# Optimization experiments

Hardware: AMD Instinct MI355X
Metric: run time of the kernel (lower is better)

Reference implementation:

```python
import jax, jax.numpy as jnp
import numpy as np

B, N, D, H, DP, DC = 1, 768, 768, 12, 128, 512
DH = D // H

def _ln(x, eps=1e-5):
    m = jnp.mean(x, axis=-1, keepdims=True)
    v = jnp.mean((x - m) ** 2, axis=-1, keepdims=True)
    return (x - m) * jax.lax.rsqrt(v + eps)

def setup_inputs() -> dict:
    key = jax.random.key(0)
    ks = jax.random.split(key, 12)
    w = lambda k, shape: jax.random.normal(k, shape, jnp.float32) * 0.02
    return dict(
        x=jax.random.normal(ks[0], (B, N, D), jnp.float32),
        pair_rep=jax.random.normal(ks[1], (B, N, N, DP), jnp.float32),
        cond=jax.random.normal(ks[2], (B, N, DC), jnp.float32),
        adaln_cond_gamma=jnp.ones((DC,), jnp.float32),
        adaln_cond_beta=jnp.zeros((DC,), jnp.float32),
        adaln_Wg=w(ks[3], (DC, D)),
        adaln_bg=jnp.zeros((D,), jnp.float32),
        adaln_Wb=w(ks[4], (DC, D)),
        Wq=w(ks[5], (D, D)), bq=jnp.zeros((D,), jnp.float32),
        Wk=w(ks[6], (D, D)), bk=jnp.zeros((D,), jnp.float32),
        Wv=w(ks[7], (D, D)), bv=jnp.zeros((D,), jnp.float32),
        qln_g=jnp.ones((DH,), jnp.float32), qln_b=jnp.zeros((DH,), jnp.float32),
        kln_g=jnp.ones((DH,), jnp.float32), kln_b=jnp.zeros((DH,), jnp.float32),
        pair_ln_g=jnp.ones((DP,), jnp.float32), pair_ln_b=jnp.zeros((DP,), jnp.float32),
        W_pair_bias=w(ks[8], (DP, H)),
        Wo=w(ks[9], (D, D)), bo=jnp.zeros((D,), jnp.float32),
        scale_W=w(ks[10], (DC, D)),
        scale_b=jnp.full((D,), -2.0, jnp.float32),  # adaLN-zero style gate bias
        mask=jnp.ones((B, N), jnp.bool_),
    )

def reference(x, pair_rep, cond, adaln_cond_gamma, adaln_cond_beta, adaln_Wg, adaln_bg,
              adaln_Wb, Wq, bq, Wk, bk, Wv, bv, qln_g, qln_b, kln_g, kln_b,
              pair_ln_g, pair_ln_b, W_pair_bias, Wo, bo, scale_W, scale_b, mask):
    b, n, d = x.shape
    mf = mask.astype(x.dtype)                      # [b, n]
    pair_mask = mf[:, :, None] * mf[:, None, :]    # [b, n, n]
    # --- AdaptiveLayerNorm: LN(x) modulated by conditioning ---
    cn = _ln(cond) * adaln_cond_gamma + adaln_cond_beta
    h = _ln(x) * jax.nn.sigmoid(cn @ adaln_Wg + adaln_bg) + cn @ adaln_Wb
    h = h * mf[..., None]
    # --- PairBiasAttention ---
    q = (h @ Wq + bq).reshape(b, n, H, DH)
    k = (h @ Wk + bk).reshape(b, n, H, DH)
    v = (h @ Wv + bv).reshape(b, n, H, DH)
    q = _ln(q) * qln_g + qln_b                     # per-head QK layernorm
    k = _ln(k) * kln_g + kln_b
    bias = (_ln(pair_rep) * pair_ln_g + pair_ln_b) @ W_pair_bias  # [b, n, n, H]
    scores = jnp.einsum('bihd,bjhd->bhij', q, k) * (1.0 / np.sqrt(DH).astype(np.float32))
    scores = scores + bias.transpose(0, 3, 1, 2)
    scores = jnp.where(pair_mask[:, None, :, :] > 0, scores, jnp.float32(-1e9))
    attn = jax.nn.softmax(scores, axis=-1)
    o = jnp.einsum('bhij,bjhd->bihd', attn, v).reshape(b, n, d)
    o = o @ Wo + bo
    # --- AdaptiveLayerNormOutputScale + final mask ---
    o = o * jax.nn.sigmoid(cond @ scale_W + scale_b) * mf[..., None]
    return o * mf[..., None]
```

## Files before the change

### kernel.cpp

```cpp
#include <hip/hip_runtime.h>
#include <math.h>

#define NN 768
#define DD 768
#define NHEAD 12
#define DPAIR 128
#define DCOND 512

typedef unsigned short u16;
typedef unsigned int u32;
typedef __attribute__((ext_vector_type(8))) short s8v;
typedef __attribute__((ext_vector_type(4))) float f4v;
#define MFMA __builtin_amdgcn_mfma_f32_16x16x32_bf16

__device__ inline u16 bf16_rne(float x) {
    u32 u = __float_as_uint(x);
    u32 r = (u + 0x7FFFu + ((u >> 16) & 1u)) >> 16;
    return (u16)r;
}
__device__ inline float bf16_f(u16 h) { return __uint_as_float(((u32)h) << 16); }
__device__ inline void split_bf16(float x, u16& hi, u16& lo) {
    hi = bf16_rne(x);
    lo = bf16_rne(x - bf16_f(hi));
}
__device__ inline u32 pk2(float a, float b) {
    return (u32)bf16_rne(a) | ((u32)bf16_rne(b) << 16);
}

struct PrepP {
    const float *pg, *pb, *Wpb, *bq, *bk, *bv, *cond, *cg, *cb, *x;
    const float* w768in[4];
    const float* w512in[3];
    u16* WpT;
    float *Av, *Bv, *bias3, *xn;
    u16 *w768oh[4], *w768ol[4], *w512oh[3], *w512ol[3];
    u16 *cnh, *cnl, *condh, *condl;
};

__device__ __forceinline__ void dev_wprep(const float* in, u16* oh, u16* ol, int K, int N,
                                          int k0, int n0) {
    __shared__ float ls[64][65];
    int t = threadIdx.x, rr = t >> 4, c4 = (t & 15) * 4;
#pragma unroll
    for (int ph = 0; ph < 4; ph++) {
        int row = ph * 16 + rr;
        float4 v = *(const float4*)(in + (long)(k0 + row) * N + n0 + c4);
        ls[c4 + 0][row] = v.x; ls[c4 + 1][row] = v.y;
        ls[c4 + 2][row] = v.z; ls[c4 + 3][row] = v.w;
    }
    __syncthreads();
#pragma unroll
    for (int ph = 0; ph < 4; ph++) {
        int row = ph * 16 + rr;
        u16 h4[4], l4[4];
#pragma unroll
        for (int i = 0; i < 4; i++) split_bf16(ls[row][c4 + i], h4[i], l4[i]);
        u32 ha = (u32)h4[0] | ((u32)h4[1] << 16), hb = (u32)h4[2] | ((u32)h4[3] << 16);
        u32 la = (u32)l4[0] | ((u32)l4[1] << 16), lb = (u32)l4[2] | ((u32)l4[3] << 16);
        long ob = (long)(n0 + row) * K + k0 + c4;
        *(uint2*)(oh + ob) = make_uint2(ha, hb);
        *(uint2*)(ol + ob) = make_uint2(la, lb);
    }
}

__device__ __forceinline__ void dev_rowln(const float* in, int C, int row,
                                          const float* g, const float* b, float* outf,
                                          u16* oh, u16* ol, u16* rawh, u16* rawl) {
    const float* x = in + (size_t)row * C;
    int t = threadIdx.x;
    float s = 0.f, s2 = 0.f;
    for (int c = t; c < C; c += 256) { float v = x[c]; s += v; s2 += v * v; }
    for (int o = 32; o > 0; o >>= 1) { s += __shfl_xor(s, o); s2 += __shfl_xor(s2, o); }
    __shared__ float r0[4], r1[4];
    int wid = t >> 6, lane = t & 63;
    if (lane == 0) { r0[wid] = s; r1[wid] = s2; }
    __syncthreads();
    s = r0[0] + r0[1] + r0[2] + r0[3];
    s2 = r1[0] + r1[1] + r1[2] + r1[3];
    float m = s / C, var = s2 / C - m * m;
    float r = rsqrtf(var + 1e-5f);
    for (int c = t; c < C; c += 256) {
        float xv = x[c];
        float v = (xv - m) * r;
        if (g) v = v * g[c] + b[c];
        size_t idx = (size_t)row * C + c;
        if (outf) outf[idx] = v;
        if (oh) { u16 hi, lo; split_bf16(v, hi, lo); oh[idx] = hi; ol[idx] = lo; }
        if (rawh) { u16 hi, lo; split_bf16(xv, hi, lo); rawh[idx] = hi; rawl[idx] = lo; }
    }
}

__global__ __launch_bounds__(256) void k_prep_all(PrepP p) {
    int bid = blockIdx.x;
    if (bid == 0) {
        int t = threadIdx.x;
        if (t < DPAIR) {
            float g = p.pg[t];
#pragma unroll
            for (int h = 0; h < 16; h++) {
                float w = (h < 12) ? g * p.Wpb[t * NHEAD + h] : 0.f;
                p.WpT[h * DPAIR + t] = bf16_rne(w);
            }
        }
        for (int idx = t; idx < 3 * DD; idx += 256) {
            float v = (idx < DD) ? p.bq[idx] : (idx < 2 * DD) ? p.bk[idx - DD] : p.bv[idx - 2 * DD];
            p.bias3[idx] = v;
        }
        if (t < NHEAD) {
            float a = 0.f, b = 0.f;
            for (int c = 0; c < DPAIR; c++) {
                a += p.pg[c] * p.Wpb[c * NHEAD + t];
                b += p.pb[c] * p.Wpb[c * NHEAD + t];
            }
            p.Av[t] = a; p.Bv[t] = b;
        }
    } else if (bid <= 576) {
        int i = bid - 1;
        dev_wprep(p.w768in[i / 144], p.w768oh[i / 144], p.w768ol[i / 144], 768, 768,
                  (i % 12) * 64, ((i / 12) % 12) * 64);
    } else if (bid <= 864) {
        int i = bid - 577;
        dev_wprep(p.w512in[i / 96], p.w512oh[i / 96], p.w512ol[i / 96], 512, 768,
                  (i & 7) * 64, ((i >> 3) % 12) * 64);
    } else if (bid <= 1632) {
        int row = bid - 865;
        dev_rowln(p.cond, 512, row, p.cg, p.cb, nullptr, p.cnh, p.cnl, p.condh, p.condl);
    } else {
        int row = bid - 1633;
        dev_rowln(p.x, 768, row, nullptr, nullptr, p.xn, nullptr, nullptr, nullptr, nullptr);
    }
}

__global__ __launch_bounds__(256) void k_pair2(const float* __restrict__ pr,
                                               const u16* __restrict__ WpT,
                                               const float* __restrict__ Av, const float* __restrict__ Bv,
                                               float* __restrict__ S) {
    __shared__ u16 At[64][128];
    __shared__ float mrow[64], rrow[64];
    long row0 = (long)blockIdx.x * 64;
    int t = threadIdx.x;
    int r = t >> 2, q = t & 3;
    const float* src = pr + (row0 + r) * DPAIR + q * 32;
    float4 v[8];
#pragma unroll
    for (int i = 0; i < 8; i++) v[i] = *(const float4*)(src + i * 4);
    float s = 0.f, s2 = 0.f;
#pragma unroll
    for (int i = 0; i < 8; i++) {
        s += v[i].x + v[i].y + v[i].z + v[i].w;
        s2 = fmaf(v[i].x, v[i].x, s2); s2 = fmaf(v[i].y, v[i].y, s2);
        s2 = fmaf(v[i].z, v[i].z, s2); s2 = fmaf(v[i].w, v[i].w, s2);
    }
    s += __shfl_xor(s, 1); s2 += __shfl_xor(s2, 1);
    s += __shfl_xor(s, 2); s2 += __shfl_xor(s2, 2);
    if (q == 0) {
        float m = s * (1.f / 128.f);
        float var = s2 * (1.f / 128.f) - m * m;
        mrow[r] = m; rrow[r] = rsqrtf(var + 1e-5f);
    }
#pragma unroll
    for (int i2 = 0; i2 < 4; i2++) {
        uint4 pk = make_uint4(pk2(v[i2 * 2].x, v[i2 * 2].y), pk2(v[i2 * 2].z, v[i2 * 2].w),
                              pk2(v[i2 * 2 + 1].x, v[i2 * 2 + 1].y), pk2(v[i2 * 2 + 1].z, v[i2 * 2 + 1].w));
        int byte = (q * 64 + i2 * 16) ^ ((r & 7) << 4);
        *(uint4*)((char*)&At[r][0] + byte) = pk;
    }
    __syncthreads();
    int w = t >> 6, l = t & 63, fr = l & 15, fq = l >> 4;
    float Ah = (fr < 12) ? Av[fr] : 0.f;
    float Bh = (fr < 12) ? Bv[fr] : 0.f;
    f4v acc = {};
#pragma unroll
    for (int ks = 0; ks < 4; ks++) {
        int arow = w * 16 + fr;
        s8v a = *(const s8v*)((char*)&At[arow][0] + ((ks * 64 + fq * 16) ^ ((arow & 7) << 4)));
        s8v b = *(const s8v*)(WpT + fr * DPAIR + ks * 32 + fq * 8);
        acc = MFMA(a, b, acc, 0, 0, 0);
    }
    if (fr < 12) {
#pragma unroll
        for (int rr = 0; rr < 4; rr++) {
            int gr = w * 16 + fq * 4 + rr;
            float bias = rrow[gr] * (acc[rr] - mrow[gr] * Ah) + Bh;
            S[(size_t)fr * (NN * NN) + row0 + gr] = bias;
        }
    }
}

__device__ __forceinline__ void gemm_phase(const u16* __restrict__ Ahp, const u16* __restrict__ Alp,
                                           const u16* __restrict__ Bhp, const u16* __restrict__ Blp,
                                           int nk, u16 (*At)[64][32], u16 (*Bt)[64][32],
                                           f4v (*acc)[2], int r, int sl, int wm, int wn,
                                           int fr, int fk) {
    uint4 ra = *(const uint4*)Ahp, rb = *(const uint4*)Alp;
    uint4 rc = *(const uint4*)Bhp, rd = *(const uint4*)Blp;
    for (int ks = 0; ks < nk; ks++) {
        *(uint4*)&At[0][r][sl * 8] = ra;
        *(uint4*)&At[1][r][sl * 8] = rb;
        *(uint4*)&Bt[0][r][sl * 8] = rc;
        *(uint4*)&Bt[1][r][sl * 8] = rd;
        __syncthreads();
        if (ks + 1 < nk) {
            int ko = (ks + 1) * 32;
            ra = *(const uint4*)(Ahp + ko); rb = *(const uint4*)(Alp + ko);
            rc = *(const uint4*)(Bhp + ko); rd = *(const uint4*)(Blp + ko);
        }
        s8v ah0 = *(const s8v*)&At[0][wm + fr][fk];
        s8v ah1 = *(const s8v*)&At[0][wm + 16 + fr][fk];
        s8v al0 = *(const s8v*)&At[1][wm + fr][fk];
        s8v al1 = *(const s8v*)&At[1][wm + 16 + fr][fk];
        s8v bh0 = *(const s8v*)&Bt[0][wn + fr][fk];
        s8v bh1 = *(const s8v*)&Bt[0][wn + 16 + fr][fk];
        s8v bl0 = *(const s8v*)&Bt[1][wn + fr][fk];
        s8v bl1 = *(const s8v*)&Bt[1][wn + 16 + fr][fk];
        acc[0][0] = MFMA(ah0, bh0, acc[0][0], 0, 0, 0);
        acc[0][0] = MFMA(ah0, bl0, acc[0][0], 0, 0, 0);
        acc[0][0] = MFMA(al0, bh0, acc[0][0], 0, 0, 0);
        acc[0][1] = MFMA(ah0, bh1, acc[0][1], 0, 0, 0);
        acc[0][1] = MFMA(ah0, bl1, acc[0][1], 0, 0, 0);
        acc[0][1] = MFMA(al0, bh1, acc[0][1], 0, 0, 0);
        acc[1][0] = MFMA(ah1, bh0, acc[1][0], 0, 0, 0);
        acc[1][0] = MFMA(ah1, bl0, acc[1][0], 0, 0, 0);
        acc[1][0] = MFMA(al1, bh0, acc[1][0], 0, 0, 0);
        acc[1][1] = MFMA(ah1, bh1, acc[1][1], 0, 0, 0);
        acc[1][1] = MFMA(ah1, bl1, acc[1][1], 0, 0, 0);
        acc[1][1] = MFMA(al1, bh1, acc[1][1], 0, 0, 0);
        __syncthreads();
    }
}

__global__ __launch_bounds__(256, 2) void k_adaln_gemm(const u16* __restrict__ Ah_, const u16* __restrict__ Al_,
                                                       const u16* __restrict__ Bgh_, const u16* __restrict__ Bgl_,
                                                       const u16* __restrict__ Bbh_, const u16* __restrict__ Bbl_,
                                                       const float* __restrict__ xn, const float* __restrict__ bg,
                                                       u16* __restrict__ hh, u16* __restrict__ hl) {
    __shared__ u16 Aa[2][64][32];
    __shared__ u16 Bb[4][64][32];
    int t = threadIdx.x;
    int m0 = blockIdx.x * 64, n0 = blockIdx.y * 64;
    int r = t >> 2, sl = t & 3;
    const u16* ap0 = Ah_ + (long)(m0 + r) * DCOND + sl * 8;
    const u16* ap1 = Al_ + (long)(m0 + r) * DCOND + sl * 8;
    const u16* bp0 = Bgh_ + (long)(n0 + r) * DCOND + sl * 8;
    const u16* bp1 = Bgl_ + (long)(n0 + r) * DCOND + sl * 8;
    const u16* bp2 = Bbh_ + (long)(n0 + r) * DCOND + sl * 8;
    const u16* bp3 = Bbl_ + (long)(n0 + r) * DCOND + sl * 8;
    int l = t & 63, w = t >> 6;
    int wm = (w >> 1) * 32, wn = (w & 1) * 32;
    int fr = l & 15, fq = l >> 4, fk = fq * 8;
    f4v ag[2][2] = {}, ab[2][2] = {};
    uint4 ra = *(const uint4*)ap0, rb = *(const uint4*)ap1;
    uint4 rc = *(const uint4*)bp0, rd = *(const uint4*)bp1;
    uint4 re = *(const uint4*)bp2, rf = *(const uint4*)bp3;
    for (int ks = 0; ks < 16; ks++) {
        *(uint4*)&Aa[0][r][sl * 8] = ra;
        *(uint4*)&Aa[1][r][sl * 8] = rb;
        *(uint4*)&Bb[0][r][sl * 8] = rc;
        *(uint4*)&Bb[1][r][sl * 8] = rd;
        *(uint4*)&Bb[2][r][sl * 8] = re;
        *(uint4*)&Bb[3][r][sl * 8] = rf;
        __syncthreads();
        if (ks + 1 < 16) {
            int ko = (ks + 1) * 32;
            ra = *(const uint4*)(ap0 + ko); rb = *(const uint4*)(ap1 + ko);
            rc = *(const uint4*)(bp0 + ko); rd = *(const uint4*)(bp1 + ko);
            re = *(const uint4*)(bp2 + ko); rf = *(const uint4*)(bp3 + ko);
        }
        s8v ah0 = *(const s8v*)&Aa[0][wm + fr][fk];
        s8v ah1 = *(const s8v*)&Aa[0][wm + 16 + fr][fk];
        s8v al0 = *(const s8v*)&Aa[1][wm + fr][fk];
        s8v al1 = *(const s8v*)&Aa[1][wm + 16 + fr][fk];
        s8v gh0 = *(const s8v*)&Bb[0][wn + fr][fk];
        s8v gh1 = *(const s8v*)&Bb[0][wn + 16 + fr][fk];
        s8v gl0 = *(const s8v*)&Bb[1][wn + fr][fk];
        s8v gl1 = *(const s8v*)&Bb[1][wn + 16 + fr][fk];
        s8v bh0 = *(const s8v*)&Bb[2][wn + fr][fk];
        s8v bh1 = *(const s8v*)&Bb[2][wn + 16 + fr][fk];
        s8v bl0 = *(const s8v*)&Bb[3][wn + fr][fk];
        s8v bl1 = *(const s8v*)&Bb[3][wn + 16 + fr][fk];
        ag[0][0] = MFMA(ah0, gh0, ag[0][0], 0, 0, 0);
        ag[0][0] = MFMA(ah0, gl0, ag[0][0], 0, 0, 0);
        ag[0][0] = MFMA(al0, gh0, ag[0][0], 0, 0, 0);
        ag[0][1] = MFMA(ah0, gh1, ag[0][1], 0, 0, 0);
        ag[0][1] = MFMA(ah0, gl1, ag[0][1], 0, 0, 0);
        ag[0][1] = MFMA(al0, gh1, ag[0][1], 0, 0, 0);
        ag[1][0] = MFMA(ah1, gh0, ag[1][0], 0, 0, 0);
        ag[1][0] = MFMA(ah1, gl0, ag[1][0], 0, 0, 0);
        ag[1][0] = MFMA(al1, gh0, ag[1][0], 0, 0, 0);
        ag[1][1] = MFMA(ah1, gh1, ag[1][1], 0, 0, 0);
        ag[1][1] = MFMA(ah1, gl1, ag[1][1], 0, 0, 0);
        ag[1][1] = MFMA(al1, gh1, ag[1][1], 0, 0, 0);
        ab[0][0] = MFMA(ah0, bh0, ab[0][0], 0, 0, 0);
        ab[0][0] = MFMA(ah0, bl0, ab[0][0], 0, 0, 0);
        ab[0][0] = MFMA(al0, bh0, ab[0][0], 0, 0, 0);
// ... 11 lines not shown
#pragma unroll
    for (int mi = 0; mi < 2; mi++)
#pragma unroll
        for (int ni = 0; ni < 2; ni++)
#pragma unroll
            for (int rr = 0; rr < 4; rr++) {
                long row = m0 + wm + mi * 16 + fq * 4 + rr;
                int col = n0 + wn + ni * 16 + fr;
                float gate = 1.f / (1.f + __expf(-(ag[mi][ni][rr] + bg[col])));
                float hv = xn[row * DD + col] * gate + ab[mi][ni][rr];
                u16 hi, lo; split_bf16(hv, hi, lo);
                hh[row * DD + col] = hi; hl[row * DD + col] = lo;
            }
}

__global__ __launch_bounds__(256, 2) void k_qkv_gemm(const u16* __restrict__ Ah_, const u16* __restrict__ Al_,
                                                     const u16* __restrict__ Wh, const u16* __restrict__ Wl,
                                                     const float* __restrict__ bias3,
                                                     const float* __restrict__ gq, const float* __restrict__ bqv,
                                                     const float* __restrict__ gk, const float* __restrict__ bkv,
                                                     u16* __restrict__ qh, u16* __restrict__ ql,
                                                     u16* __restrict__ kh, u16* __restrict__ vth) {
    __shared__ u16 At[2][64][32], Bt[2][64][32];
    __shared__ float redS[2][64], redS2[2][64];
    int t = threadIdx.x;
    int m0 = blockIdx.x * 64, n0 = blockIdx.y * 64, z = blockIdx.z;
    int r = t >> 2, sl = t & 3;
    const u16* Ahp = Ah_ + (long)(m0 + r) * DD + sl * 8;
    const u16* Alp = Al_ + (long)(m0 + r) * DD + sl * 8;
    const u16* Bhp = Wh + (long)z * 589824 + (long)(n0 + r) * DD + sl * 8;
    const u16* Blp = Wl + (long)z * 589824 + (long)(n0 + r) * DD + sl * 8;
    int l = t & 63, w = t >> 6;
    int wm = (w >> 1) * 32, wn = (w & 1) * 32;
    int fr = l & 15, fq = l >> 4, fk = fq * 8;
    f4v acc[2][2] = {};
    gemm_phase(Ahp, Alp, Bhp, Blp, 24, At, Bt, acc, r, sl, wm, wn, fr, fk);
    float vv[2][2][4];
#pragma unroll
    for (int mi = 0; mi < 2; mi++)
#pragma unroll
        for (int ni = 0; ni < 2; ni++)
#pragma unroll
            for (int rr = 0; rr < 4; rr++)
                vv[mi][ni][rr] = acc[mi][ni][rr] + bias3[z * DD + n0 + wn + ni * 16 + fr];
    if (z == 2) {
#pragma unroll
        for (int mi = 0; mi < 2; mi++)
#pragma unroll
            for (int ni = 0; ni < 2; ni++)
#pragma unroll
                for (int rr = 0; rr < 4; rr++) {
// ... 4 lines not shown
        return;
    }
    int wi = w & 1;
#pragma unroll
    for (int mi = 0; mi < 2; mi++)
#pragma unroll
        for (int rr = 0; rr < 4; rr++) {
            float sv = vv[mi][0][rr] + vv[mi][1][rr];
            float s2v = vv[mi][0][rr] * vv[mi][0][rr] + vv[mi][1][rr] * vv[mi][1][rr];
            sv += __shfl_xor(sv, 1); s2v += __shfl_xor(s2v, 1);
            sv += __shfl_xor(sv, 2); s2v += __shfl_xor(s2v, 2);
            sv += __shfl_xor(sv, 4); s2v += __shfl_xor(s2v, 4);
            sv += __shfl_xor(sv, 8); s2v += __shfl_xor(s2v, 8);
            if (fr == 0) {
                int row = wm + mi * 16 + fq * 4 + rr;
                redS[wi][row] = sv; redS2[wi][row] = s2v;
            }
        }
    __syncthreads();
    const float* g = z ? gk : gq;
    const float* bb = z ? bkv : bqv;
    float scale = z ? 1.f : 0.125f;
#pragma unroll
    for (int mi = 0; mi < 2; mi++)
#pragma unroll
        for (int ni = 0; ni < 2; ni++)
#pragma unroll
            for (int rr = 0; rr < 4; rr++) {
                int row = wm + mi * 16 + fq * 4 + rr;
                float m = (redS[0][row] + redS[1][row]) * (1.f / 64.f);
                float var = (redS2[0][row] + redS2[1][row]) * (1.f / 64.f) - m * m;
                float rs = rsqrtf(var + 1e-5f);
                int colh = wn + ni * 16 + fr;
                float y = ((vv[mi][ni][rr] - m) * rs * g[colh] + bb[colh]) * scale;
                size_t idx = (size_t)(m0 + row) * DD + n0 + colh;
                if (z == 0) { u16 hi, lo; split_bf16(y, hi, lo); qh[idx] = hi; ql[idx] = lo; }
                else kh[idx] = bf16_rne(y);
            }
}

__global__ __launch_bounds__(128) void k_flash(const u16* __restrict__ qh, const u16* __restrict__ ql,
                                               const u16* __restrict__ kh, const u16* __restrict__ vt,
                                               const float* __restrict__ S,
                                               u16* __restrict__ oh, u16* __restrict__ ol) {
    __shared__ u16 Kt[64][64];
    __shared__ u16 Vt[64][64];
    __shared__ u16 Pt[2][16][72];
    int i0 = blockIdx.x * 32, h = blockIdx.y;
    int t = threadIdx.x, w = t >> 6, l = t & 63, fr = l & 15, fq = l >> 4;
    const u16* qsrc = qh + (size_t)(i0 + w * 16 + fr) * DD + h * 64 + fq * 8;
    const u16* qsrc2 = ql + (size_t)(i0 + w * 16 + fr) * DD + h * 64 + fq * 8;
    s8v qa0 = *(const s8v*)qsrc, qa1 = *(const s8v*)(qsrc + 32);
    s8v qb0 = *(const s8v*)qsrc2, qb1 = *(const s8v*)(qsrc2 + 32);
// ... 29 lines not shown
            sc[nf] = MFMA(qb0, kb0, sc[nf], 0, 0, 0);
            sc[nf] = MFMA(qa1, kb1, sc[nf], 0, 0, 0);
            sc[nf] = MFMA(qb1, kb1, sc[nf], 0, 0, 0);
        }
#pragma unroll
        for (int rr = 0; rr < 4; rr++) {
            float mx = fmaxf(fmaxf(sc[0][rr], sc[1][rr]), fmaxf(sc[2][rr], sc[3][rr]));
            mx = fmaxf(mx, __shfl_xor(mx, 1));
            mx = fmaxf(mx, __shfl_xor(mx, 2));
            mx = fmaxf(mx, __shfl_xor(mx, 4));
            mx = fmaxf(mx, __shfl_xor(mx, 8));
            float mnew = fmaxf(mrun[rr], mx);
            float ps = 0.f;
#pragma unroll
            for (int nf = 0; nf < 4; nf++) {
                float p = __expf(sc[nf][rr] - mnew);
                sc[nf][rr] = p;
                ps += p;
            }
            ps += __shfl_xor(ps, 1); ps += __shfl_xor(ps, 2);
            ps += __shfl_xor(ps, 4); ps += __shfl_xor(ps, 8);
            float f = __expf(mrun[rr] - mnew);
            lrun[rr] = lrun[rr] * f + ps;
            mrun[rr] = mnew;
#pragma unroll
            for (int nf = 0; nf < 4; nf++) Oacc[nf][rr] *= f;
        }
#pragma unroll
        for (int nf = 0; nf < 4; nf++)
#pragma unroll
            for (int rr = 0; rr < 4; rr++)
                Pt[w][fq * 4 + rr][nf * 16 + fr] = bf16_rne(sc[nf][rr]);
#pragma unroll
// ... 7 lines not shown
            }
        }
        __syncthreads();
    }
#pragma unroll
    for (int rr = 0; rr < 4; rr++) lrun[rr] = 1.f / lrun[rr];
#pragma unroll
    for (int nf = 0; nf < 4; nf++)
#pragma unroll
        for (int rr = 0; rr < 4; rr++) {
            float o = Oacc[nf][rr] * lrun[rr];
            u16 hi, lo; split_bf16(o, hi, lo);
            size_t idx = (size_t)(i0 + w * 16 + fq * 4 + rr) * DD + h * 64 + nf * 16 + fr;
            oh[idx] = hi; ol[idx] = lo;
        }
}

__global__ __launch_bounds__(256, 2) void k_out_gemm(const u16* __restrict__ oh_, const u16* __restrict__ ol_,
                                                     const u16* __restrict__ Woh, const u16* __restrict__ Wol,
                                                     const u16* __restrict__ ch, const u16* __restrict__ cl,
                                                     const u16* __restrict__ sWh, const u16* __restrict__ sWl,
                                                     const float* __restrict__ bo, const float* __restrict__ sb,
                                                     float* __restrict__ outp) {
    __shared__ u16 At[2][64][32], Bt[2][64][32];
    int t = threadIdx.x;
    int m0 = blockIdx.x * 64, n0 = blockIdx.y * 64;
    int r = t >> 2, sl = t & 3;
    int l = t & 63, w = t >> 6;
    int wm = (w >> 1) * 32, wn = (w & 1) * 32;
    int fr = l & 15, fq = l >> 4, fk = fq * 8;
// ... 62 lines not shown
    u16* condl = up; up += E5;
    u16* hh = up; up += E;
    u16* hl = up; up += E;
    u16* qh = up; up += E;
    u16* ql = up; up += E;
    u16* kh = up; up += E;
    u16* vth = up; up += E;
    u16* WT768h = up; up += 4 * E;
    u16* WT768l = up; up += 4 * E;
    u16* WT512h = up; up += 3 * E5;
    u16* WT512l = up; up += 3 * E5;
    u16* WpT = up; up += 2048;

    float* out = (float*)d_out;

    PrepP P;
    P.pg = pg; P.pb = pb; P.Wpb = Wpb; P.bq = bq; P.bk = bk; P.bv = bv;
    P.cond = cond; P.cg = cg; P.cb = cb; P.x = x;
    P.w768in[0] = Wq; P.w768in[1] = Wk; P.w768in[2] = Wv; P.w768in[3] = Wo;
    P.w512in[0] = Wg; P.w512in[1] = Wb; P.w512in[2] = sW;
    P.WpT = WpT; P.Av = Av; P.Bv = Bv; P.bias3 = bias3; P.xn = xn;
    for (int i = 0; i < 4; i++) { P.w768oh[i] = WT768h + i * E; P.w768ol[i] = WT768l + i * E; }
    for (int i = 0; i < 3; i++) { P.w512oh[i] = WT512h + i * E5; P.w512ol[i] = WT512l + i * E5; }
    P.cnh = cnh; P.cnl = cnl; P.condh = condh; P.condl = condl;

    k_prep_all<<<2401, 256, 0, stream>>>(P);
    k_pair2<<<9216, 256, 0, stream>>>(pair, WpT, Av, Bv, S);
    k_adaln_gemm<<<dim3(12, 12), 256, 0, stream>>>(cnh, cnl, WT512h, WT512l,
                                                   WT512h + E5, WT512l + E5, xn, bg, hh, hl);
    k_qkv_gemm<<<dim3(12, 12, 3), 256, 0, stream>>>(hh, hl, WT768h, WT768l, bias3,
                                                    qln_g, qln_b, kln_g, kln_b, qh, ql, kh, vth);
    k_flash<<<dim3(24, 12), 128, 0, stream>>>(qh, ql, kh, vth, S, qh, ql);
    k_out_gemm<<<dim3(12, 12), 256, 0, stream>>>(qh, ql, WT768h + 3 * E, WT768l + 3 * E,
                                                 condh, condl, WT512h + 2 * E5, WT512l + 2 * E5,
                                                 bo, sb, out);
}
```

Measured before the change: 213.4 us.

## Co-schedule pair-bias blocks with prep, adaLN and QKV GEMM launches

The 9216 pair-bias blocks are split across three fused launches (1800, 3400 and 4016 blocks). Each share runs alongside the weight-prep/LN stage, the adaLN GEMM and the QKV GEMM, using block-index dispatch and a shared-memory union. The aim is to fill idle compute units during the small GEMM launches with bandwidth-heavy pair work, and to drop one kernel launch. It adds a tiny separate prep0 launch that must finish first. Launch bounds of 2 blocks per SM and the larger shared-memory union may reduce occupancy for the pair blocks.

Result: faster. 189.9 us (-11.0%).

```diff
diff --git a/kernel.cpp b/kernel.cpp
--- a/kernel.cpp
+++ b/kernel.cpp
@@ -27,26 +27,99 @@
     return (u32)bf16_rne(a) | ((u32)bf16_rne(b) << 16);
 }
 
-struct PrepP {
-    const float *pg, *pb, *Wpb, *bq, *bk, *bv, *cond, *cg, *cb, *x;
-    const float* w768in[4];
-    const float* w512in[3];
-    u16* WpT;
-    float *Av, *Bv, *bias3, *xn;
-    u16 *w768oh[4], *w768ol[4], *w512oh[3], *w512ol[3];
-    u16 *cnh, *cnl, *condh, *condl;
-};
+struct SmPair { u16 At[64][128]; float mrow[64]; float rrow[64]; };
+struct SmW    { float ls[64][65]; float r0[4]; float r1[4]; };
+struct SmAda  { u16 Aa[2][64][32]; u16 Bb[4][64][32]; };
+struct SmQkv  { u16 At[2][64][32]; u16 Bt[2][64][32]; float redS[2][64]; float redS2[2][64]; };
+
+__global__ void k_prep0(const float* __restrict__ pg, const float* __restrict__ pb,
+                        const float* __restrict__ W, u16* __restrict__ WpT,
+                        float* __restrict__ Av, float* __restrict__ Bv,
+                        const float* __restrict__ bq, const float* __restrict__ bk,
+                        const float* __restrict__ bv, float* __restrict__ bias3) {
+    int t = threadIdx.x;
+    if (t < DPAIR) {
+        float g = pg[t];
+#pragma unroll
+        for (int h = 0; h < 16; h++) {
+            float w = (h < 12) ? g * W[t * NHEAD + h] : 0.f;
+            WpT[h * DPAIR + t] = bf16_rne(w);
+        }
+    }
+    for (int idx = t; idx < 3 * DD; idx += 256) {
+        float v = (idx < DD) ? bq[idx] : (idx < 2 * DD) ? bk[idx - DD] : bv[idx - 2 * DD];
+        bias3[idx] = v;
+    }
+    if (t < NHEAD) {
+        float a = 0.f, b = 0.f;
+        for (int c = 0; c < DPAIR; c++) { a += pg[c] * W[c * NHEAD + t]; b += pb[c] * W[c * NHEAD + t]; }
+        Av[t] = a; Bv[t] = b;
+    }
+}
+
+__device__ __forceinline__ void dev_pair(int unit, SmPair& sm, const float* __restrict__ pr,
+                                         const u16* __restrict__ WpT,
+                                         const float* __restrict__ Av, const float* __restrict__ Bv,
+                                         float* __restrict__ S) {
+    long row0 = (long)unit * 64;
+    int t = threadIdx.x;
+    int r = t >> 2, q = t & 3;
+    const float* src = pr + (row0 + r) * DPAIR + q * 32;
+    float4 v[8];
+#pragma unroll
+    for (int i = 0; i < 8; i++) v[i] = *(const float4*)(src + i * 4);
+    float s = 0.f, s2 = 0.f;
+#pragma unroll
+    for (int i = 0; i < 8; i++) {
+        s += v[i].x + v[i].y + v[i].z + v[i].w;
+        s2 = fmaf(v[i].x, v[i].x, s2); s2 = fmaf(v[i].y, v[i].y, s2);
+        s2 = fmaf(v[i].z, v[i].z, s2); s2 = fmaf(v[i].w, v[i].w, s2);
+    }
+    s += __shfl_xor(s, 1); s2 += __shfl_xor(s2, 1);
+    s += __shfl_xor(s, 2); s2 += __shfl_xor(s2, 2);
+    if (q == 0) {
+        float m = s * (1.f / 128.f);
+        float var = s2 * (1.f / 128.f) - m * m;
+        sm.mrow[r] = m; sm.rrow[r] = rsqrtf(var + 1e-5f);
+    }
+#pragma unroll
+    for (int i2 = 0; i2 < 4; i2++) {
+        uint4 pk = make_uint4(pk2(v[i2 * 2].x, v[i2 * 2].y), pk2(v[i2 * 2].z, v[i2 * 2].w),
+                              pk2(v[i2 * 2 + 1].x, v[i2 * 2 + 1].y), pk2(v[i2 * 2 + 1].z, v[i2 * 2 + 1].w));
+        int byte = (q * 64 + i2 * 16) ^ ((r & 7) << 4);
+        *(uint4*)((char*)&sm.At[r][0] + byte) = pk;
+    }
+    __syncthreads();
+    int w = t >> 6, l = t & 63, fr = l & 15, fq = l >> 4;
+    float Ah = (fr < 12) ? Av[fr] : 0.f;
+    float Bh = (fr < 12) ? Bv[fr] : 0.f;
+    f4v acc = {};
+#pragma unroll
+    for (int ks = 0; ks < 4; ks++) {
+        int arow = w * 16 + fr;
+        s8v a = *(const s8v*)((char*)&sm.At[arow][0] + ((ks * 64 + fq * 16) ^ ((arow & 7) << 4)));
+        s8v b = *(const s8v*)(WpT + fr * DPAIR + ks * 32 + fq * 8);
+        acc = MFMA(a, b, acc, 0, 0, 0);
+    }
+    if (fr < 12) {
+#pragma unroll
+        for (int rr = 0; rr < 4; rr++) {
+            int gr = w * 16 + fq * 4 + rr;
+            float bias = sm.rrow[gr] * (acc[rr] - sm.mrow[gr] * Ah) + Bh;
+            S[(size_t)fr * (NN * NN) + row0 + gr] = bias;
+        }
+    }
+}
 
 __device__ __forceinline__ void dev_wprep(const float* in, u16* oh, u16* ol, int K, int N,
-                                          int k0, int n0) {
-    __shared__ float ls[64][65];
+                                          int k0, int n0, SmW& sm) {
     int t = threadIdx.x, rr = t >> 4, c4 = (t & 15) * 4;
 #pragma unroll
     for (int ph = 0; ph < 4; ph++) {
         int row = ph * 16 + rr;
         float4 v = *(const float4*)(in + (long)(k0 + row) * N + n0 + c4);
-        ls[c4 + 0][row] = v.x; ls[c4 + 1][row] = v.y;
-        ls[c4 + 2][row] = v.z; ls[c4 + 3][row] = v.w;
+        sm.ls[c4 + 0][row] = v.x; sm.ls[c4 + 1][row] = v.y;
+        sm.ls[c4 + 2][row] = v.z; sm.ls[c4 + 3][row] = v.w;
     }
     __syncthreads();
 #pragma unroll
@@ -54,7 +127,7 @@
         int row = ph * 16 + rr;
         u16 h4[4], l4[4];
 #pragma unroll
-        for (int i = 0; i < 4; i++) split_bf16(ls[row][c4 + i], h4[i], l4[i]);
+        for (int i = 0; i < 4; i++) split_bf16(sm.ls[row][c4 + i], h4[i], l4[i]);
         u32 ha = (u32)h4[0] | ((u32)h4[1] << 16), hb = (u32)h4[2] | ((u32)h4[3] << 16);
         u32 la = (u32)l4[0] | ((u32)l4[1] << 16), lb = (u32)l4[2] | ((u32)l4[3] << 16);
         long ob = (long)(n0 + row) * K + k0 + c4;
@@ -65,18 +138,17 @@
 
 __device__ __forceinline__ void dev_rowln(const float* in, int C, int row,
                                           const float* g, const float* b, float* outf,
-                                          u16* oh, u16* ol, u16* rawh, u16* rawl) {
+                                          u16* oh, u16* ol, u16* rawh, u16* rawl, SmW& sm) {
     const float* x = in + (size_t)row * C;
     int t = threadIdx.x;
     float s = 0.f, s2 = 0.f;
     for (int c = t; c < C; c += 256) { float v = x[c]; s += v; s2 += v * v; }
     for (int o = 32; o > 0; o >>= 1) { s += __shfl_xor(s, o); s2 += __shfl_xor(s2, o); }
-    __shared__ float r0[4], r1[4];
     int wid = t >> 6, lane = t & 63;
-    if (lane == 0) { r0[wid] = s; r1[wid] = s2; }
+    if (lane == 0) { sm.r0[wid] = s; sm.r1[wid] = s2; }
     __syncthreads();
-    s = r0[0] + r0[1] + r0[2] + r0[3];
-    s2 = r1[0] + r1[1] + r1[2] + r1[3];
+    s = sm.r0[0] + sm.r0[1] + sm.r0[2] + sm.r0[3];
+    s2 = sm.r1[0] + sm.r1[1] + sm.r1[2] + sm.r1[3];
     float m = s / C, var = s2 / C - m * m;
     float r = rsqrtf(var + 1e-5f);
     for (int c = t; c < C; c += 256) {
@@ -90,154 +162,14 @@
     }
 }
 
-__global__ __launch_bounds__(256) void k_prep_all(PrepP p) {
-    int bid = blockIdx.x;
-    if (bid == 0) {
-        int t = threadIdx.x;
-        if (t < DPAIR) {
-            float g = p.pg[t];
-#pragma unroll
-            for (int h = 0; h < 16; h++) {
-                float w = (h < 12) ? g * p.Wpb[t * NHEAD + h] : 0.f;
-                p.WpT[h * DPAIR + t] = bf16_rne(w);
-            }
-        }
-        for (int idx = t; idx < 3 * DD; idx += 256) {
-            float v = (idx < DD) ? p.bq[idx] : (idx < 2 * DD) ? p.bk[idx - DD] : p.bv[idx - 2 * DD];
-            p.bias3[idx] = v;
-        }
-        if (t < NHEAD) {
-            float a = 0.f, b = 0.f;
-            for (int c = 0; c < DPAIR; c++) {
-                a += p.pg[c] * p.Wpb[c * NHEAD + t];
-                b += p.pb[c] * p.Wpb[c * NHEAD + t];
-            }
-            p.Av[t] = a; p.Bv[t] = b;
-        }
-    } else if (bid <= 576) {
-        int i = bid - 1;
-        dev_wprep(p.w768in[i / 144], p.w768oh[i / 144], p.w768ol[i / 144], 768, 768,
-                  (i % 12) * 64, ((i / 12) % 12) * 64);
-    } else if (bid <= 864) {
-        int i = bid - 577;
-        dev_wprep(p.w512in[i / 96], p.w512oh[i / 96], p.w512ol[i / 96], 512, 768,
-                  (i & 7) * 64, ((i >> 3) % 12) * 64);
-    } else if (bid <= 1632) {
-        int row = bid - 865;
-        dev_rowln(p.cond, 512, row, p.cg, p.cb, nullptr, p.cnh, p.cnl, p.condh, p.condl);
-    } else {
-        int row = bid - 1633;
-        dev_rowln(p.x, 768, row, nullptr, nullptr, p.xn, nullptr, nullptr, nullptr, nullptr);
-    }
-}
-
-__global__ __launch_bounds__(256) void k_pair2(const float* __restrict__ pr,
-                                               const u16* __restrict__ WpT,
-                                               const float* __restrict__ Av, const float* __restrict__ Bv,
-                                               float* __restrict__ S) {
-    __shared__ u16 At[64][128];
-    __shared__ float mrow[64], rrow[64];
-    long row0 = (long)blockIdx.x * 64;
+__device__ __forceinline__ void dev_adaln(int bx, int by, SmAda& sm,
+                                          const u16* __restrict__ Ah_, const u16* __restrict__ Al_,
+                                          const u16* __restrict__ Bgh_, const u16* __restrict__ Bgl_,
+                                          const u16* __restrict__ Bbh_, const u16* __restrict__ Bbl_,
+                                          const float* __restrict__ xn, const float* __restrict__ bg,
+                                          u16* __restrict__ hh, u16* __restrict__ hl) {
     int t = threadIdx.x;
-    int r = t >> 2, q = t & 3;
-    const float* src = pr + (row0 + r) * DPAIR + q * 32;
-    float4 v[8];
-#pragma unroll
-    for (int i = 0; i < 8; i++) v[i] = *(const float4*)(src + i * 4);
-    float s = 0.f, s2 = 0.f;
-#pragma unroll
-    for (int i = 0; i < 8; i++) {
-        s += v[i].x + v[i].y + v[i].z + v[i].w;
-        s2 = fmaf(v[i].x, v[i].x, s2); s2 = fmaf(v[i].y, v[i].y, s2);
-        s2 = fmaf(v[i].z, v[i].z, s2); s2 = fmaf(v[i].w, v[i].w, s2);
-    }
-    s += __shfl_xor(s, 1); s2 += __shfl_xor(s2, 1);
-    s += __shfl_xor(s, 2); s2 += __shfl_xor(s2, 2);
-    if (q == 0) {
-        float m = s * (1.f / 128.f);
-        float var = s2 * (1.f / 128.f) - m * m;
-        mrow[r] = m; rrow[r] = rsqrtf(var + 1e-5f);
-    }
-#pragma unroll
-    for (int i2 = 0; i2 < 4; i2++) {
-        uint4 pk = make_uint4(pk2(v[i2 * 2].x, v[i2 * 2].y), pk2(v[i2 * 2].z, v[i2 * 2].w),
-                              pk2(v[i2 * 2 + 1].x, v[i2 * 2 + 1].y), pk2(v[i2 * 2 + 1].z, v[i2 * 2 + 1].w));
-        int byte = (q * 64 + i2 * 16) ^ ((r & 7) << 4);
-        *(uint4*)((char*)&At[r][0] + byte) = pk;
-    }
-    __syncthreads();
-    int w = t >> 6, l = t & 63, fr = l & 15, fq = l >> 4;
-    float Ah = (fr < 12) ? Av[fr] : 0.f;
-    float Bh = (fr < 12) ? Bv[fr] : 0.f;
-    f4v acc = {};
-#pragma unroll
-    for (int ks = 0; ks < 4; ks++) {
-        int arow = w * 16 + fr;
-        s8v a = *(const s8v*)((char*)&At[arow][0] + ((ks * 64 + fq * 16) ^ ((arow & 7) << 4)));
-        s8v b = *(const s8v*)(WpT + fr * DPAIR + ks * 32 + fq * 8);
-        acc = MFMA(a, b, acc, 0, 0, 0);
-    }
-    if (fr < 12) {
-#pragma unroll
-        for (int rr = 0; rr < 4; rr++) {
-            int gr = w * 16 + fq * 4 + rr;
-            float bias = rrow[gr] * (acc[rr] - mrow[gr] * Ah) + Bh;
-            S[(size_t)fr * (NN * NN) + row0 + gr] = bias;
-        }
-    }
-}
-
-__device__ __forceinline__ void gemm_phase(const u16* __restrict__ Ahp, const u16* __restrict__ Alp,
-                                           const u16* __restrict__ Bhp, const u16* __restrict__ Blp,
-                                           int nk, u16 (*At)[64][32], u16 (*Bt)[64][32],
-                                           f4v (*acc)[2], int r, int sl, int wm, int wn,
-                                           int fr, int fk) {
-    uint4 ra = *(const uint4*)Ahp, rb = *(const uint4*)Alp;
-    uint4 rc = *(const uint4*)Bhp, rd = *(const uint4*)Blp;
-    for (int ks = 0; ks < nk; ks++) {
-        *(uint4*)&At[0][r][sl * 8] = ra;
-        *(uint4*)&At[1][r][sl * 8] = rb;
-        *(uint4*)&Bt[0][r][sl * 8] = rc;
-        *(uint4*)&Bt[1][r][sl * 8] = rd;
-        __syncthreads();
-        if (ks + 1 < nk) {
-            int ko = (ks + 1) * 32;
-            ra = *(const uint4*)(Ahp + ko); rb = *(const uint4*)(Alp + ko);
-            rc = *(const uint4*)(Bhp + ko); rd = *(const uint4*)(Blp + ko);
-        }
-        s8v ah0 = *(const s8v*)&At[0][wm + fr][fk];
-        s8v ah1 = *(const s8v*)&At[0][wm + 16 + fr][fk];
-        s8v al0 = *(const s8v*)&At[1][wm + fr][fk];
-        s8v al1 = *(const s8v*)&At[1][wm + 16 + fr][fk];
-        s8v bh0 = *(const s8v*)&Bt[0][wn + fr][fk];
-        s8v bh1 = *(const s8v*)&Bt[0][wn + 16 + fr][fk];
-        s8v bl0 = *(const s8v*)&Bt[1][wn + fr][fk];
-        s8v bl1 = *(const s8v*)&Bt[1][wn + 16 + fr][fk];
-        acc[0][0] = MFMA(ah0, bh0, acc[0][0], 0, 0, 0);
-        acc[0][0] = MFMA(ah0, bl0, acc[0][0], 0, 0, 0);
-        acc[0][0] = MFMA(al0, bh0, acc[0][0], 0, 0, 0);
-        acc[0][1] = MFMA(ah0, bh1, acc[0][1], 0, 0, 0);
-        acc[0][1] = MFMA(ah0, bl1, acc[0][1], 0, 0, 0);
-        acc[0][1] = MFMA(al0, bh1, acc[0][1], 0, 0, 0);
-        acc[1][0] = MFMA(ah1, bh0, acc[1][0], 0, 0, 0);
-        acc[1][0] = MFMA(ah1, bl0, acc[1][0], 0, 0, 0);
-        acc[1][0] = MFMA(al1, bh0, acc[1][0], 0, 0, 0);
-        acc[1][1] = MFMA(ah1, bh1, acc[1][1], 0, 0, 0);
-        acc[1][1] = MFMA(ah1, bl1, acc[1][1], 0, 0, 0);
-        acc[1][1] = MFMA(al1, bh1, acc[1][1], 0, 0, 0);
-        __syncthreads();
-    }
-}
-
-__global__ __launch_bounds__(256, 2) void k_adaln_gemm(const u16* __restrict__ Ah_, const u16* __restrict__ Al_,
-                                                       const u16* __restrict__ Bgh_, const u16* __restrict__ Bgl_,
-                                                       const u16* __restrict__ Bbh_, const u16* __restrict__ Bbl_,
-                                                       const float* __restrict__ xn, const float* __restrict__ bg,
-                                                       u16* __restrict__ hh, u16* __restrict__ hl) {
-    __shared__ u16 Aa[2][64][32];
-    __shared__ u16 Bb[4][64][32];
-    int t = threadIdx.x;
-    int m0 = blockIdx.x * 64, n0 = blockIdx.y * 64;
+    int m0 = bx * 64, n0 = by * 64;
     int r = t >> 2, sl = t & 3;
     const u16* ap0 = Ah_ + (long)(m0 + r) * DCOND + sl * 8;
     const u16* ap1 = Al_ + (long)(m0 + r) * DCOND + sl * 8;
@@ -253,12 +185,12 @@
     uint4 rc = *(const uint4*)bp0, rd = *(const uint4*)bp1;
     uint4 re = *(const uint4*)bp2, rf = *(const uint4*)bp3;
     for (int ks = 0; ks < 16; ks++) {
-        *(uint4*)&Aa[0][r][sl * 8] = ra;
-        *(uint4*)&Aa[1][r][sl * 8] = rb;
-        *(uint4*)&Bb[0][r][sl * 8] = rc;
-        *(uint4*)&Bb[1][r][sl * 8] = rd;
-        *(uint4*)&Bb[2][r][sl * 8] = re;
-        *(uint4*)&Bb[3][r][sl * 8] = rf;
+        *(uint4*)&sm.Aa[0][r][sl * 8] = ra;
+        *(uint4*)&sm.Aa[1][r][sl * 8] = rb;
+        *(uint4*)&sm.Bb[0][r][sl * 8] = rc;
+        *(uint4*)&sm.Bb[1][r][sl * 8] = rd;
+        *(uint4*)&sm.Bb[2][r][sl * 8] = re;
+        *(uint4*)&sm.Bb[3][r][sl * 8] = rf;
         __syncthreads();
         if (ks + 1 < 16) {
             int ko = (ks + 1) * 32;
@@ -266,18 +198,18 @@
             rc = *(const uint4*)(bp0 + ko); rd = *(const uint4*)(bp1 + ko);
             re = *(const uint4*)(bp2 + ko); rf = *(const uint4*)(bp3 + ko);
         }
-        s8v ah0 = *(const s8v*)&Aa[0][wm + fr][fk];
-        s8v ah1 = *(const s8v*)&Aa[0][wm + 16 + fr][fk];
-        s8v al0 = *(const s8v*)&Aa[1][wm + fr][fk];
-        s8v al1 = *(const s8v*)&Aa[1][wm + 16 + fr][fk];
-        s8v gh0 = *(const s8v*)&Bb[0][wn + fr][fk];
-        s8v gh1 = *(const s8v*)&Bb[0][wn + 16 + fr][fk];
-        s8v gl0 = *(const s8v*)&Bb[1][wn + fr][fk];
-        s8v gl1 = *(const s8v*)&Bb[1][wn + 16 + fr][fk];
-        s8v bh0 = *(const s8v*)&Bb[2][wn + fr][fk];
-        s8v bh1 = *(const s8v*)&Bb[2][wn + 16 + fr][fk];
-        s8v bl0 = *(const s8v*)&Bb[3][wn + fr][fk];
-        s8v bl1 = *(const s8v*)&Bb[3][wn + 16 + fr][fk];
+        s8v ah0 = *(const s8v*)&sm.Aa[0][wm + fr][fk];
+        s8v ah1 = *(const s8v*)&sm.Aa[0][wm + 16 + fr][fk];
+        s8v al0 = *(const s8v*)&sm.Aa[1][wm + fr][fk];
+        s8v al1 = *(const s8v*)&sm.Aa[1][wm + 16 + fr][fk];
+        s8v gh0 = *(const s8v*)&sm.Bb[0][wn + fr][fk];
+        s8v gh1 = *(const s8v*)&sm.Bb[0][wn + 16 + fr][fk];
+        s8v gl0 = *(const s8v*)&sm.Bb[1][wn + fr][fk];
+        s8v gl1 = *(const s8v*)&sm.Bb[1][wn + 16 + fr][fk];
+        s8v bh0 = *(const s8v*)&sm.Bb[2][wn + fr][fk];
+        s8v bh1 = *(const s8v*)&sm.Bb[2][wn + 16 + fr][fk];
+        s8v bl0 = *(const s8v*)&sm.Bb[3][wn + fr][fk];
+        s8v bl1 = *(const s8v*)&sm.Bb[3][wn + 16 + fr][fk];
         ag[0][0] = MFMA(ah0, gh0, ag[0][0], 0, 0, 0);
         ag[0][0] = MFMA(ah0, gl0, ag[0][0], 0, 0, 0);
         ag[0][0] = MFMA(al0, gh0, ag[0][0], 0, 0, 0);
@@ -319,17 +251,16 @@
             }
 }
 
-__global__ __launch_bounds__(256, 2) void k_qkv_gemm(const u16* __restrict__ Ah_, const u16* __restrict__ Al_,
-                                                     const u16* __restrict__ Wh, const u16* __restrict__ Wl,
-                                                     const float* __restrict__ bias3,
-                                                     const float* __restrict__ gq, const float* __restrict__ bqv,
-                                                     const float* __restrict__ gk, const float* __restrict__ bkv,
-                                                     u16* __restrict__ qh, u16* __restrict__ ql,
-                                                     u16* __restrict__ kh, u16* __restrict__ vth) {
-    __shared__ u16 At[2][64][32], Bt[2][64][32];
-    __shared__ float redS[2][64], redS2[2][64];
+__device__ __forceinline__ void dev_qkv(int bx, int by, int z, SmQkv& sm,
+                                        const u16* __restrict__ Ah_, const u16* __restrict__ Al_,
+                                        const u16* __restrict__ Wh, const u16* __restrict__ Wl,
+                                        const float* __restrict__ bias3,
+                                        const float* __restrict__ gq, const float* __restrict__ bqv,
+                                        const float* __restrict__ gk, const float* __restrict__ bkv,
+                                        u16* __restrict__ qh, u16* __restrict__ ql,
+                                        u16* __restrict__ kh, u16* __restrict__ vth) {
     int t = threadIdx.x;
-    int m0 = blockIdx.x * 64, n0 = blockIdx.y * 64, z = blockIdx.z;
+    int m0 = bx * 64, n0 = by * 64;
     int r = t >> 2, sl = t & 3;
     const u16* Ahp = Ah_ + (long)(m0 + r) * DD + sl * 8;
     const u16* Alp = Al_ + (long)(m0 + r) * DD + sl * 8;
@@ -339,7 +270,43 @@
     int wm = (w >> 1) * 32, wn = (w & 1) * 32;
     int fr = l & 15, fq = l >> 4, fk = fq * 8;
     f4v acc[2][2] = {};
-    gemm_phase(Ahp, Alp, Bhp, Blp, 24, At, Bt, acc, r, sl, wm, wn, fr, fk);
+    {
+        uint4 ra = *(const uint4*)Ahp, rb = *(const uint4*)Alp;
+        uint4 rc = *(const uint4*)Bhp, rd = *(const uint4*)Blp;
+        for (int ks = 0; ks < 24; ks++) {
+            *(uint4*)&sm.At[0][r][sl * 8] = ra;
+            *(uint4*)&sm.At[1][r][sl * 8] = rb;
+            *(uint4*)&sm.Bt[0][r][sl * 8] = rc;
+            *(uint4*)&sm.Bt[1][r][sl * 8] = rd;
+            __syncthreads();
+            if (ks + 1 < 24) {
+                int ko = (ks + 1) * 32;
+                ra = *(const uint4*)(Ahp + ko); rb = *(const uint4*)(Alp + ko);
+                rc = *(const uint4*)(Bhp + ko); rd = *(const uint4*)(Blp + ko);
+            }
+            s8v ah0 = *(const s8v*)&sm.At[0][wm + fr][fk];
+            s8v ah1 = *(const s8v*)&sm.At[0][wm + 16 + fr][fk];
+            s8v al0 = *(const s8v*)&sm.At[1][wm + fr][fk];
+            s8v al1 = *(const s8v*)&sm.At[1][wm + 16 + fr][fk];
+            s8v bh0 = *(const s8v*)&sm.Bt[0][wn + fr][fk];
+            s8v bh1 = *(const s8v*)&sm.Bt[0][wn + 16 + fr][fk];
+            s8v bl0 = *(const s8v*)&sm.Bt[1][wn + fr][fk];
+            s8v bl1 = *(const s8v*)&sm.Bt[1][wn + 16 + fr][fk];
+            acc[0][0] = MFMA(ah0, bh0, acc[0][0], 0, 0, 0);
+            acc[0][0] = MFMA(ah0, bl0, acc[0][0], 0, 0, 0);
+            acc[0][0] = MFMA(al0, bh0, acc[0][0], 0, 0, 0);
+            acc[0][1] = MFMA(ah0, bh1, acc[0][1], 0, 0, 0);
+            acc[0][1] = MFMA(ah0, bl1, acc[0][1], 0, 0, 0);
+            acc[0][1] = MFMA(al0, bh1, acc[0][1], 0, 0, 0);
+            acc[1][0] = MFMA(ah1, bh0, acc[1][0], 0, 0, 0);
+            acc[1][0] = MFMA(ah1, bl0, acc[1][0], 0, 0, 0);
+            acc[1][0] = MFMA(al1, bh0, acc[1][0], 0, 0, 0);
+            acc[1][1] = MFMA(ah1, bh1, acc[1][1], 0, 0, 0);
+            acc[1][1] = MFMA(ah1, bl1, acc[1][1], 0, 0, 0);
+            acc[1][1] = MFMA(al1, bh1, acc[1][1], 0, 0, 0);
+            __syncthreads();
+        }
+    }
     float vv[2][2][4];
 #pragma unroll
     for (int mi = 0; mi < 2; mi++)
@@ -374,7 +341,7 @@
             sv += __shfl_xor(sv, 8); s2v += __shfl_xor(s2v, 8);
             if (fr == 0) {
                 int row = wm + mi * 16 + fq * 4 + rr;
-                redS[wi][row] = sv; redS2[wi][row] = s2v;
+                sm.redS[wi][row] = sv; sm.redS2[wi][row] = s2v;
             }
         }
     __syncthreads();
@@ -388,8 +355,8 @@
 #pragma unroll
             for (int rr = 0; rr < 4; rr++) {
                 int row = wm + mi * 16 + fq * 4 + rr;
-                float m = (redS[0][row] + redS[1][row]) * (1.f / 64.f);
-                float var = (redS2[0][row] + redS2[1][row]) * (1.f / 64.f) - m * m;
+                float m = (sm.redS[0][row] + sm.redS[1][row]) * (1.f / 64.f);
+                float var = (sm.redS2[0][row] + sm.redS2[1][row]) * (1.f / 64.f) - m * m;
                 float rs = rsqrtf(var + 1e-5f);
                 int colh = wn + ni * 16 + fr;
                 float y = ((vv[mi][ni][rr] - m) * rs * g[colh] + bb[colh]) * scale;
@@ -397,6 +364,70 @@
                 if (z == 0) { u16 hi, lo; split_bf16(y, hi, lo); qh[idx] = hi; ql[idx] = lo; }
                 else kh[idx] = bf16_rne(y);
             }
+}
+
+struct L1P {
+    const float* w768in[4]; u16* w768oh[4]; u16* w768ol[4];
+    const float* w512in[3]; u16* w512oh[3]; u16* w512ol[3];
+    const float *cond, *cg, *cb, *x;
+    u16 *cnh, *cnl, *condh, *condl; float* xn;
+    const float* pr; const u16* WpT; const float *Av, *Bv; float* S;
+};
+__global__ __launch_bounds__(256, 2) void k_L1(L1P p) {
+    __shared__ __align__(16) char smraw[(sizeof(SmPair) > sizeof(SmW)) ? sizeof(SmPair) : sizeof(SmW)];
+    int bid = blockIdx.x;
+    if (bid < 576) {
+        int i = bid;
+        dev_wprep(p.w768in[i / 144], p.w768oh[i / 144], p.w768ol[i / 144], 768, 768,
+                  (i % 12) * 64, ((i / 12) % 12) * 64, *(SmW*)smraw);
+    } else if (bid < 864) {
+        int i = bid - 576;
+        dev_wprep(p.w512in[i / 96], p.w512oh[i / 96], p.w512ol[i / 96], 512, 768,
+                  (i & 7) * 64, ((i >> 3) % 12) * 64, *(SmW*)smraw);
+    } else if (bid < 1632) {
+        dev_rowln(p.cond, 512, bid - 864, p.cg, p.cb, nullptr, p.cnh, p.cnl, p.condh, p.condl, *(SmW*)smraw);
+    } else if (bid < 2400) {
+        dev_rowln(p.x, 768, bid - 1632, nullptr, nullptr, p.xn, nullptr, nullptr, nullptr, nullptr, *(SmW*)smraw);
+    } else {
+        dev_pair(bid - 2400, *(SmPair*)smraw, p.pr, p.WpT, p.Av, p.Bv, p.S);
+    }
+}
+
+struct L2P {
+    const u16 *cnh, *cnl, *WT512h, *WT512l;
+    const float *xn, *bg; u16 *hh, *hl;
+    const float* pr; const u16* WpT; const float *Av, *Bv; float* S;
+    int pairBase;
+};
+__global__ __launch_bounds__(256, 2) void k_L2(L2P p) {
+    __shared__ __align__(16) char smraw[(sizeof(SmAda) > sizeof(SmPair)) ? sizeof(SmAda) : sizeof(SmPair)];
+    int bid = blockIdx.x;
+    if (bid < 144) {
+        dev_adaln(bid % 12, bid / 12, *(SmAda*)smraw, p.cnh, p.cnl,
+                  p.WT512h, p.WT512l, p.WT512h + 393216, p.WT512l + 393216,
+                  p.xn, p.bg, p.hh, p.hl);
+    } else {
+        dev_pair(p.pairBase + bid - 144, *(SmPair*)smraw, p.pr, p.WpT, p.Av, p.Bv, p.S);
+    }
+}
+
+struct L3P {
+    const u16 *hh, *hl, *WT768h, *WT768l;
+    const float *bias3, *gq, *bqv, *gk, *bkv;
+    u16 *qh, *ql, *kh, *vth;
+    const float* pr; const u16* WpT; const float *Av, *Bv; float* S;
+    int pairBase;
+};
+__global__ __launch_bounds__(256, 2) void k_L3(L3P p) {
+    __shared__ __align__(16) char smraw[(sizeof(SmQkv) > sizeof(SmPair)) ? sizeof(SmQkv) : sizeof(SmPair)];
+    int bid = blockIdx.x;
+    if (bid < 432) {
+        int z = bid / 144, rem = bid % 144;
+        dev_qkv(rem % 12, rem / 12, z, *(SmQkv*)smraw, p.hh, p.hl, p.WT768h, p.WT768l,
+                p.bias3, p.gq, p.bqv, p.gk, p.bkv, p.qh, p.ql, p.kh, p.vth);
+    } else {
+        dev_pair(p.pairBase + bid - 432, *(SmPair*)smraw, p.pr, p.WpT, p.Av, p.Bv, p.S);
+    }
 }
 
 __global__ __launch_bounds__(128) void k_flash(const u16* __restrict__ qh, const u16* __restrict__ ql,
@@ -456,9 +487,9 @@
             float ps = 0.f;
 #pragma unroll
             for (int nf = 0; nf < 4; nf++) {
-                float p = __expf(sc[nf][rr] - mnew);
-                sc[nf][rr] = p;
-                ps += p;
+                float pv = __expf(sc[nf][rr] - mnew);
+                sc[nf][rr] = pv;
+                ps += pv;
             }
             ps += __shfl_xor(ps, 1); ps += __shfl_xor(ps, 2);
             ps += __shfl_xor(ps, 4); ps += __shfl_xor(ps, 8);
@@ -496,6 +527,48 @@
             size_t idx = (size_t)(i0 + w * 16 + fq * 4 + rr) * DD + h * 64 + nf * 16 + fr;
             oh[idx] = hi; ol[idx] = lo;
         }
+}
+
+__device__ __forceinline__ void gemm_phase(const u16* __restrict__ Ahp, const u16* __restrict__ Alp,
+                                           const u16* __restrict__ Bhp, const u16* __restrict__ Blp,
+                                           int nk, u16 (*At)[64][32], u16 (*Bt)[64][32],
+                                           f4v (*acc)[2], int r, int sl, int wm, int wn,
+                                           int fr, int fk) {
+    uint4 ra = *(const uint4*)Ahp, rb = *(const uint4*)Alp;
+    uint4 rc = *(const uint4*)Bhp, rd = *(const uint4*)Blp;
+    for (int ks = 0; ks < nk; ks++) {
+        *(uint4*)&At[0][r][sl * 8] = ra;
+        *(uint4*)&At[1][r][sl * 8] = rb;
+        *(uint4*)&Bt[0][r][sl * 8] = rc;
+        *(uint4*)&Bt[1][r][sl * 8] = rd;
+        __syncthreads();
+        if (ks + 1 < nk) {
+            int ko = (ks + 1) * 32;
+            ra = *(const uint4*)(Ahp + ko); rb = *(const uint4*)(Alp + ko);
+            rc = *(const uint4*)(Bhp + ko); rd = *(const uint4*)(Blp + ko);
+        }
+        s8v ah0 = *(const s8v*)&At[0][wm + fr][fk];
+        s8v ah1 = *(const s8v*)&At[0][wm + 16 + fr][fk];
+        s8v al0 = *(const s8v*)&At[1][wm + fr][fk];
+        s8v al1 = *(const s8v*)&At[1][wm + 16 + fr][fk];
+        s8v bh0 = *(const s8v*)&Bt[0][wn + fr][fk];
+        s8v bh1 = *(const s8v*)&Bt[0][wn + 16 + fr][fk];
+        s8v bl0 = *(const s8v*)&Bt[1][wn + fr][fk];
+        s8v bl1 = *(const s8v*)&Bt[1][wn + 16 + fr][fk];
+        acc[0][0] = MFMA(ah0, bh0, acc[0][0], 0, 0, 0);
+        acc[0][0] = MFMA(ah0, bl0, acc[0][0], 0, 0, 0);
+        acc[0][0] = MFMA(al0, bh0, acc[0][0], 0, 0, 0);
+        acc[0][1] = MFMA(ah0, bh1, acc[0][1], 0, 0, 0);
+        acc[0][1] = MFMA(ah0, bl1, acc[0][1], 0, 0, 0);
+        acc[0][1] = MFMA(al0, bh1, acc[0][1], 0, 0, 0);
+        acc[1][0] = MFMA(ah1, bh0, acc[1][0], 0, 0, 0);
+        acc[1][0] = MFMA(ah1, bl0, acc[1][0], 0, 0, 0);
+        acc[1][0] = MFMA(al1, bh0, acc[1][0], 0, 0, 0);
+        acc[1][1] = MFMA(ah1, bh1, acc[1][1], 0, 0, 0);
+        acc[1][1] = MFMA(ah1, bl1, acc[1][1], 0, 0, 0);
+        acc[1][1] = MFMA(al1, bh1, acc[1][1], 0, 0, 0);
+        __syncthreads();
+    }
 }
 
 __global__ __launch_bounds__(256, 2) void k_out_gemm(const u16* __restrict__ oh_, const u16* __restrict__ ol_,
@@ -588,23 +661,35 @@
 
     float* out = (float*)d_out;
 
-    PrepP P;
-    P.pg = pg; P.pb = pb; P.Wpb = Wpb; P.bq = bq; P.bk = bk; P.bv = bv;
-    P.cond = cond; P.cg = cg; P.cb = cb; P.x = x;
-    P.w768in[0] = Wq; P.w768in[1] = Wk; P.w768in[2] = Wv; P.w768in[3] = Wo;
-    P.w512in[0] = Wg; P.w512in[1] = Wb; P.w512in[2] = sW;
-    P.WpT = WpT; P.Av = Av; P.Bv = Bv; P.bias3 = bias3; P.xn = xn;
-    for (int i = 0; i < 4; i++) { P.w768oh[i] = WT768h + i * E; P.w768ol[i] = WT768l + i * E; }
-    for (int i = 0; i < 3; i++) { P.w512oh[i] = WT512h + i * E5; P.w512ol[i] = WT512l + i * E5; }
-    P.cnh = cnh; P.cnl = cnl; P.condh = condh; P.condl = condl;
-
-    k_prep_all<<<2401, 256, 0, stream>>>(P);
-    k_pair2<<<9216, 256, 0, stream>>>(pair, WpT, Av, Bv, S);
-    k_adaln_gemm<<<dim3(12, 12), 256, 0, stream>>>(cnh, cnl, WT512h, WT512l,
-                                                   WT512h + E5, WT512l + E5, xn, bg, hh, hl);
-    k_qkv_gemm<<<dim3(12, 12, 3), 256, 0, stream>>>(hh, hl, WT768h, WT768l, bias3,
-                                                    qln_g, qln_b, kln_g, kln_b, qh, ql, kh, vth);
+    k_prep0<<<1, 256, 0, stream>>>(pg, pb, Wpb, WpT, Av, Bv, bq, bk, bv, bias3);
+
+    L1P p1;
+    p1.w768in[0] = Wq; p1.w768in[1] = Wk; p1.w768in[2] = Wv; p1.w768in[3] = Wo;
+    for (int i = 0; i < 4; i++) { p1.w768oh[i] = WT768h + i * E; p1.w768ol[i] = WT768l + i * E; }
+    p1.w512in[0] = Wg; p1.w512in[1] = Wb; p1.w512in[2] = sW;
+    for (int i = 0; i < 3; i++) { p1.w512oh[i] = WT512h + i * E5; p1.w512ol[i] = WT512l + i * E5; }
+    p1.cond = cond; p1.cg = cg; p1.cb = cb; p1.x = x;
+    p1.cnh = cnh; p1.cnl = cnl; p1.condh = condh; p1.condl = condl; p1.xn = xn;
+    p1.pr = pair; p1.WpT = WpT; p1.Av = Av; p1.Bv = Bv; p1.S = S;
+    k_L1<<<2400 + 1800, 256, 0, stream>>>(p1);
+
+    L2P p2;
+    p2.cnh = cnh; p2.cnl = cnl; p2.WT512h = WT512h; p2.WT512l = WT512l;
+    p2.xn = xn; p2.bg = bg; p2.hh = hh; p2.hl = hl;
+    p2.pr = pair; p2.WpT = WpT; p2.Av = Av; p2.Bv = Bv; p2.S = S;
+    p2.pairBase = 1800;
+    k_L2<<<144 + 3400, 256, 0, stream>>>(p2);
+
+    L3P p3;
+    p3.hh = hh; p3.hl = hl; p3.WT768h = WT768h; p3.WT768l = WT768l;
+    p3.bias3 = bias3; p3.gq = qln_g; p3.bqv = qln_b; p3.gk = kln_g; p3.bkv = kln_b;
+    p3.qh = qh; p3.ql = ql; p3.kh = kh; p3.vth = vth;
+    p3.pr = pair; p3.WpT = WpT; p3.Av = Av; p3.Bv = Bv; p3.S = S;
+    p3.pairBase = 5200;
+    k_L3<<<432 + 4016, 256, 0, stream>>>(p3);
+
     k_flash<<<dim3(24, 12), 128, 0, stream>>>(qh, ql, kh, vth, S, qh, ql);
+
     k_out_gemm<<<dim3(12, 12), 256, 0, stream>>>(qh, ql, WT768h + 3 * E, WT768l + 3 * E,
                                                  condh, condl, WT512h + 2 * E5, WT512l + 2 * E5,
                                                  bo, sb, out);
```
